# Kernel optimization log

Measured on AMD Instinct MI355X. Metric: run time of the kernel, lower is better.

Reference implementation:

```python
import jax, jax.numpy as jnp
import numpy as np

PROB_THRESHOLD = 0.5


def setup_inputs() -> dict:
    key = jax.random.key(0)
    B, H, W = 64, 480, 864
    mask = jax.random.uniform(key, (B, H, W), dtype=jnp.float32)
    return {"mask": mask, "n_pts_threshold": 10, "n_bbox_loose_pixels": 64}


def reference(mask, n_pts_threshold, n_bbox_loose_pixels):
    """Threshold mask, find per-sample bbox of above-threshold pixels, loosen
    by n_bbox_loose_pixels, and emit a binary attention map over that bbox.
    If fewer than n_pts_threshold pixels fire, the whole frame is attended.
    Returns (att_map [B,H,W] float, bbox [B,4] int32 as [y0,y1,x0,x1])."""
    B, H, W = mask.shape
    binm = mask > PROB_THRESHOLD                       # [B,H,W] bool
    cnt = jnp.sum(binm, axis=(1, 2))                   # [B]

    rows = jnp.any(binm, axis=2)                       # [B,H] row has a hit
    cols = jnp.any(binm, axis=1)                       # [B,W] col has a hit
    r_idx = jnp.arange(H, dtype=jnp.int32)
    c_idx = jnp.arange(W, dtype=jnp.int32)

    min_r = jnp.min(jnp.where(rows, r_idx, H), axis=1)
    max_r = jnp.max(jnp.where(rows, r_idx, -1), axis=1)
    min_c = jnp.min(jnp.where(cols, c_idx, W), axis=1)
    max_c = jnp.max(jnp.where(cols, c_idx, -1), axis=1)

    loose = jnp.int32(n_bbox_loose_pixels)
    full = cnt < n_pts_threshold                       # too few pts -> full frame
    y0 = jnp.where(full, 0,     jnp.clip(min_r - loose, 0, H - 1))
    y1 = jnp.where(full, H - 1, jnp.clip(max_r + loose, 0, H - 1))
    x0 = jnp.where(full, 0,     jnp.clip(min_c - loose, 0, W - 1))
    x1 = jnp.where(full, W - 1, jnp.clip(max_c + loose, 0, W - 1))

    in_rows = (r_idx[None, :] >= y0[:, None]) & (r_idx[None, :] <= y1[:, None])  # [B,H]
    in_cols = (c_idx[None, :] >= x0[:, None]) & (c_idx[None, :] <= x1[:, None])  # [B,W]
    att_map = (in_rows[:, :, None] & in_cols[:, None, :]).astype(mask.dtype)     # [B,H,W]

    bbox = jnp.stack([y0, y1, x0, x1], axis=1).astype(jnp.int32)                 # [B,4]
    return att_map, bbox
```

## Files before the change

### kernel.cpp

```cpp
#include <hip/hip_runtime.h>

constexpr int B = 64;
constexpr int H = 480;
constexpr int W = 864;
constexpr float PROB_THRESHOLD = 0.5f;

constexpr int BPS = 16;
constexpr int ROWS_PER_BLK = H / BPS;
constexpr int W4 = W / 4;
constexpr int N4_PER_BLK = ROWS_PER_BLK * W4;
constexpr int NBLK = B * BPS;
constexpr int NPAIRS = ROWS_PER_BLK / 2;

using f32x4 = __attribute__((ext_vector_type(4))) float;
using u64 = unsigned long long;

constexpr u64 MARKER = 0xFFull << 56;

__device__ inline u64 pack_partial(int minr, int maxr, int minc, int maxc,
                                   int cnt) {
  u64 v = (u64)(unsigned)minr | ((u64)(unsigned)(maxr + 1) << 9) |
          ((u64)(unsigned)minc << 18) | ((u64)(unsigned)(maxc + 1) << 28) |
          ((u64)(unsigned)min(cnt, 4095) << 38) | MARKER;
  return v;
}

__global__ __launch_bounds__(256, 4) void fused_kernel(
    const float* __restrict__ mask, const int* __restrict__ n_pts_threshold,
    const int* __restrict__ n_bbox_loose, float* __restrict__ out,
    float* __restrict__ bbox_out, u64* __restrict__ part) {
  const int b    = blockIdx.x >> 4;
  const int blk  = blockIdx.x & 15;
  const int row0 = blk * ROWS_PER_BLK;
  const f32x4* __restrict__ m4 =
      (const f32x4*)(mask + ((size_t)b * H + row0) * (size_t)W);

  const int thr = n_pts_threshold[0];
  const int tid = threadIdx.x;
  const int wave = tid >> 6;
  const int lane = tid & 63;

  const bool aTop = tid < W4;
  const int aC4   = aTop ? tid : tid - W4;
  const bool hasB = tid < (2 * W4 - 256);
  const int bC4   = tid + (256 - W4);
  const int aC = aC4 * 4, bC = bC4 * 4;

  int minr = H, maxr = -1, minc = W, maxc = -1, cnt = 0;

  auto proc = [&](f32x4 v, int row, int c) {
    bool h0 = v.x > PROB_THRESHOLD;
    bool h1 = v.y > PROB_THRESHOLD;
    bool h2 = v.z > PROB_THRESHOLD;
    bool h3 = v.w > PROB_THRESHOLD;
    int m = (h0 ? 1 : 0) | (h1 ? 2 : 0) | (h2 ? 4 : 0) | (h3 ? 8 : 0);
    if (m) {
      minr = min(minr, row);
      maxr = max(maxr, row);
      minc = min(minc, c + (__ffs(m) - 1));
      maxc = max(maxc, c + (31 - __clz(m)));
      cnt += __popc(m);
    }
  };

  auto loadA = [&](int s) {
    int rr = aTop ? s : (ROWS_PER_BLK - 1 - s);
    return __builtin_nontemporal_load(&m4[rr * W4 + aC4]);
  };
  auto loadB = [&](int s) {
    return __builtin_nontemporal_load(&m4[(ROWS_PER_BLK - 1 - s) * W4 + bC4]);
  };

  __shared__ int rflags[4];
  __shared__ int rcnt[4];
  __shared__ int s5[4][5];
  __shared__ u64 packed[BPS];

  bool stopped = false;
  f32x4 pa = loadA(0);
  f32x4 pb{};
  if (hasB) pb = loadB(0);

  for (int s = 0; s < NPAIRS; ++s) {
    f32x4 ca = pa, cb = pb;
    const int sn = (s + 1 < NPAIRS) ? s + 1 : s;
    pa = loadA(sn);
    if (hasB) pb = loadB(sn);

    const int rt = row0 + s;
    const int rb = row0 + ROWS_PER_BLK - 1 - s;
    proc(ca, aTop ? rt : rb, aC);
    if (hasB) proc(cb, rb, bC);

    int wc = cnt;
    for (int off = 1; off < 64; off <<= 1) wc += __shfl_xor(wc, off);
    int fl = (__any(minr == row0) ? 1 : 0) |
             (__any(maxr == row0 + ROWS_PER_BLK - 1) ? 2 : 0) |
             (__any(minc == 0) ? 4 : 0) |
             (__any(maxc == W - 1) ? 8 : 0);
    if (lane == 0) { rflags[wave] = fl; rcnt[wave] = wc; }
    __syncthreads();
    const int bfl  = rflags[0] | rflags[1] | rflags[2] | rflags[3];
    const int bcnt = rcnt[0] + rcnt[1] + rcnt[2] + rcnt[3];
    const bool stop = (bfl == 15) && (bcnt >= thr);
    __syncthreads();
    if (stop) { stopped = true; break; }
  }

  u64* __restrict__ P = part + (size_t)b * BPS;
  if (stopped) {
    if (tid == 0)
      __hip_atomic_store(
          &P[blk],
          pack_partial(row0, row0 + ROWS_PER_BLK - 1, 0, W - 1, 4095),
          __ATOMIC_RELAXED, __HIP_MEMORY_SCOPE_AGENT);
  } else {
    for (int off = 32; off > 0; off >>= 1) {
      minr = min(minr, __shfl_down(minr, off));
      maxr = max(maxr, __shfl_down(maxr, off));
      minc = min(minc, __shfl_down(minc, off));
      maxc = max(maxc, __shfl_down(maxc, off));
      cnt += __shfl_down(cnt, off);
    }
    if (lane == 0) {
      s5[wave][0] = minr; s5[wave][1] = maxr;
      s5[wave][2] = minc; s5[wave][3] = maxc;
      s5[wave][4] = cnt;
    }
    __syncthreads();
    if (tid == 0) {
      for (int wv = 1; wv < 4; ++wv) {
        minr = min(minr, s5[wv][0]);
        maxr = max(maxr, s5[wv][1]);
        minc = min(minc, s5[wv][2]);
        maxc = max(maxc, s5[wv][3]);
        cnt += s5[wv][4];
      }
      __hip_atomic_store(&P[blk], pack_partial(minr, maxr, minc, maxc, cnt),
                         __ATOMIC_RELAXED, __HIP_MEMORY_SCOPE_AGENT);
    }
  }

  if (tid < BPS) {
    u64 v;
    while (((v = __hip_atomic_load(&P[tid], __ATOMIC_RELAXED,
                                   __HIP_MEMORY_SCOPE_AGENT)) >> 56) != 0xFF)
      __builtin_amdgcn_s_sleep(2);
    packed[tid] = v;
  }
  __syncthreads();

  minr = H; maxr = -1; minc = W; maxc = -1; cnt = 0;
#pragma unroll
  for (int k = 0; k < BPS; ++k) {
    u64 v = packed[k];
    minr = min(minr, (int)(v & 511));
    maxr = max(maxr, (int)((v >> 9) & 511) - 1);
    minc = min(minc, (int)((v >> 18) & 1023));
    maxc = max(maxc, (int)((v >> 28) & 1023) - 1);
    cnt += (int)((v >> 38) & 4095);
  }
  const int loose = n_bbox_loose[0];
  int y0, y1, x0, x1;
  if (cnt < thr) {
    y0 = 0; y1 = H - 1; x0 = 0; x1 = W - 1;
  } else {
    y0 = min(max(minr - loose, 0), H - 1);
    y1 = min(max(maxr + loose, 0), H - 1);
    x0 = min(max(minc - loose, 0), W - 1);
    x1 = min(max(maxc + loose, 0), W - 1);
  }
  if (blk == 0 && tid == 0) {
    bbox_out[b * 4 + 0] = (float)y0;
    bbox_out[b * 4 + 1] = (float)y1;
    bbox_out[b * 4 + 2] = (float)x0;
    bbox_out[b * 4 + 3] = (float)x1;
  }

  f32x4* obase = (f32x4*)(out + ((size_t)b * H + row0) * (size_t)W);

  auto val4 = [&](int i2) {
    int r = i2 / W4;
    int c = (i2 - r * W4) * 4;
    int rr = row0 + r;
    bool inr = (rr >= y0) & (rr <= y1);
    f32x4 v;
    v.x = (inr & (c + 0 >= x0) & (c + 0 <= x1)) ? 1.0f : 0.0f;
    v.y = (inr & (c + 1 >= x0) & (c + 1 <= x1)) ? 1.0f : 0.0f;
    v.z = (inr & (c + 2 >= x0) & (c + 2 <= x1)) ? 1.0f : 0.0f;
    v.w = (inr & (c + 3 >= x0) & (c + 3 <= x1)) ? 1.0f : 0.0f;
    return v;
  };

  int i = tid;
  for (int it = 0; it < 6; ++it, i += 1024) {
    __builtin_nontemporal_store(val4(i),       &obase[i]);
    __builtin_nontemporal_store(val4(i + 256), &obase[i + 256]);
    __builtin_nontemporal_store(val4(i + 512), &obase[i + 512]);
    __builtin_nontemporal_store(val4(i + 768), &obase[i + 768]);
  }
  __builtin_nontemporal_store(val4(i), &obase[i]);
  i += 256;
  if (i < N4_PER_BLK) __builtin_nontemporal_store(val4(i), &obase[i]);
}

extern "C" void kernel_launch(void* const* d_in, const int* in_sizes, int n_in,
                              void* d_out, int out_size, void* d_ws,
                              size_t ws_size, hipStream_t stream) {
  const float* mask = (const float*)d_in[0];
  const int* n_pts_threshold = (const int*)d_in[1];
  const int* n_bbox_loose = (const int*)d_in[2];

  float* out = (float*)d_out;
  float* bbox_out = out + (size_t)B * H * W;
  u64* part = (u64*)d_ws;

  fused_kernel<<<NBLK, 256, 0, stream>>>(mask, n_pts_threshold, n_bbox_loose,
                                         out, bbox_out, part);
}
```

Before: 167.9 us.

## Double-buffer stop-check flags, peel first step, precompute column mask for writes

The early-exit vote now uses ping-pong shared arrays indexed by step parity, which removes the second __syncthreads per iteration. The first row pair is peeled so a block can stop before issuing the next prefetch. The output write computes each thread's column mask once and streams whole rows, choosing between that mask and zeros per row, which avoids the per-element divide and compare work. The write loop only uses the 216 threads that have a column, so 40 threads sit idle during the store phase.

```diff
diff --git a/kernel.cpp b/kernel.cpp
--- a/kernel.cpp
+++ b/kernel.cpp
@@ -71,40 +71,48 @@
     return __builtin_nontemporal_load(&m4[(ROWS_PER_BLK - 1 - s) * W4 + bC4]);
   };
 
-  __shared__ int rflags[4];
-  __shared__ int rcnt[4];
+  __shared__ int vfl[2][4];
+  __shared__ int vcn[2][4];
   __shared__ int s5[4][5];
   __shared__ u64 packed[BPS];
 
-  bool stopped = false;
-  f32x4 pa = loadA(0);
-  f32x4 pb{};
-  if (hasB) pb = loadB(0);
-
-  for (int s = 0; s < NPAIRS; ++s) {
-    f32x4 ca = pa, cb = pb;
-    const int sn = (s + 1 < NPAIRS) ? s + 1 : s;
-    pa = loadA(sn);
-    if (hasB) pb = loadB(sn);
-
-    const int rt = row0 + s;
-    const int rb = row0 + ROWS_PER_BLK - 1 - s;
-    proc(ca, aTop ? rt : rb, aC);
-    if (hasB) proc(cb, rb, bC);
-
+  auto stopCheck = [&](int s) -> bool {
     int wc = cnt;
     for (int off = 1; off < 64; off <<= 1) wc += __shfl_xor(wc, off);
     int fl = (__any(minr == row0) ? 1 : 0) |
              (__any(maxr == row0 + ROWS_PER_BLK - 1) ? 2 : 0) |
              (__any(minc == 0) ? 4 : 0) |
              (__any(maxc == W - 1) ? 8 : 0);
-    if (lane == 0) { rflags[wave] = fl; rcnt[wave] = wc; }
+    const int p = s & 1;
+    if (lane == 0) { vfl[p][wave] = fl; vcn[p][wave] = wc; }
     __syncthreads();
-    const int bfl  = rflags[0] | rflags[1] | rflags[2] | rflags[3];
-    const int bcnt = rcnt[0] + rcnt[1] + rcnt[2] + rcnt[3];
-    const bool stop = (bfl == 15) && (bcnt >= thr);
-    __syncthreads();
-    if (stop) { stopped = true; break; }
+    const int bfl  = vfl[p][0] | vfl[p][1] | vfl[p][2] | vfl[p][3];
+    const int bcnt = vcn[p][0] + vcn[p][1] + vcn[p][2] + vcn[p][3];
+    return (bfl == 15) & (bcnt >= thr);
+  };
+
+  bool stopped;
+  {
+    f32x4 ca = loadA(0), cb{};
+    if (hasB) cb = loadB(0);
+    proc(ca, aTop ? row0 : row0 + ROWS_PER_BLK - 1, aC);
+    if (hasB) proc(cb, row0 + ROWS_PER_BLK - 1, bC);
+    stopped = stopCheck(0);
+  }
+  if (!stopped) {
+    f32x4 pa = loadA(1), pb{};
+    if (hasB) pb = loadB(1);
+    for (int s = 1; s < NPAIRS; ++s) {
+      f32x4 ca = pa, cb = pb;
+      const int sn = (s + 1 < NPAIRS) ? s + 1 : s;
+      pa = loadA(sn);
+      if (hasB) pb = loadB(sn);
+      const int rt = row0 + s;
+      const int rb = row0 + ROWS_PER_BLK - 1 - s;
+      proc(ca, aTop ? rt : rb, aC);
+      if (hasB) proc(cb, rb, bC);
+      if ((stopped = stopCheck(s))) break;
+    }
   }
 
   u64* __restrict__ P = part + (size_t)b * BPS;
@@ -177,31 +185,23 @@
     bbox_out[b * 4 + 3] = (float)x1;
   }
 
-  f32x4* obase = (f32x4*)(out + ((size_t)b * H + row0) * (size_t)W);
-
-  auto val4 = [&](int i2) {
-    int r = i2 / W4;
-    int c = (i2 - r * W4) * 4;
-    int rr = row0 + r;
-    bool inr = (rr >= y0) & (rr <= y1);
-    f32x4 v;
-    v.x = (inr & (c + 0 >= x0) & (c + 0 <= x1)) ? 1.0f : 0.0f;
-    v.y = (inr & (c + 1 >= x0) & (c + 1 <= x1)) ? 1.0f : 0.0f;
-    v.z = (inr & (c + 2 >= x0) & (c + 2 <= x1)) ? 1.0f : 0.0f;
-    v.w = (inr & (c + 3 >= x0) & (c + 3 <= x1)) ? 1.0f : 0.0f;
-    return v;
-  };
-
-  int i = tid;
-  for (int it = 0; it < 6; ++it, i += 1024) {
-    __builtin_nontemporal_store(val4(i),       &obase[i]);
-    __builtin_nontemporal_store(val4(i + 256), &obase[i + 256]);
-    __builtin_nontemporal_store(val4(i + 512), &obase[i + 512]);
-    __builtin_nontemporal_store(val4(i + 768), &obase[i + 768]);
-  }
-  __builtin_nontemporal_store(val4(i), &obase[i]);
-  i += 256;
-  if (i < N4_PER_BLK) __builtin_nontemporal_store(val4(i), &obase[i]);
+  if (tid < W4) {
+    const int c = tid * 4;
+    f32x4 colv, zero;
+    colv.x = ((c + 0 >= x0) & (c + 0 <= x1)) ? 1.0f : 0.0f;
+    colv.y = ((c + 1 >= x0) & (c + 1 <= x1)) ? 1.0f : 0.0f;
+    colv.z = ((c + 2 >= x0) & (c + 2 <= x1)) ? 1.0f : 0.0f;
+    colv.w = ((c + 3 >= x0) & (c + 3 <= x1)) ? 1.0f : 0.0f;
+    zero.x = 0.0f; zero.y = 0.0f; zero.z = 0.0f; zero.w = 0.0f;
+
+    f32x4* p = (f32x4*)(out + ((size_t)b * H + row0) * (size_t)W) + tid;
+    int rr = row0;
+#pragma unroll
+    for (int r = 0; r < ROWS_PER_BLK; ++r, ++rr, p += W4) {
+      const bool inr = (rr >= y0) & (rr <= y1);
+      __builtin_nontemporal_store(inr ? colv : zero, p);
+    }
+  }
 }
 
 extern "C" void kernel_launch(void* const* d_in, const int* in_sizes, int n_in,
```

New measurement: 167.1 us (median of 2 runs). About the same (-0.5%).
